# Performance work log

Hardware: AMD Instinct MI355X
Metric: run time of the kernel (lower is better)

Reference implementation:

```python
import jax, jax.numpy as jnp
import numpy as np

EPS = 1e-8  # torch F.cosine_similarity eps


def setup_inputs() -> dict:
    key = jax.random.key(0)
    B, CAP, CD, CTX = 32, 32768, 64, 64
    ks = jax.random.split(key, 9)
    inp = {
        "query_content": jax.random.normal(ks[0], (B, CD), jnp.float32),
        "query_context": jax.random.normal(ks[1], (B, CTX), jnp.float32),
        "memory_content": 0.1 * jax.random.normal(ks[2], (CAP, CD), jnp.float32),
        "memory_contexts": 0.1 * jax.random.normal(ks[3], (CAP, CTX), jnp.float32),
        "memory_freshness": jnp.ones((CAP,), jnp.float32),
        "W1": jax.random.normal(ks[4], (2 * CD, CD), jnp.float32) / np.sqrt(2 * CD),
        "b1": 0.01 * jax.random.normal(ks[5], (CD,), jnp.float32),
        "W2": jax.random.normal(ks[6], (CD, 1), jnp.float32) / np.sqrt(CD),
        "b2": 0.01 * jax.random.normal(ks[7], (1,), jnp.float32),
        "top_k": 16,
    }
    return inp


def reference(query_content, query_context, memory_content, memory_contexts,
              memory_freshness, W1, b1, W2, b2, top_k):
    B, CD = query_content.shape
    # similarity_calculator MLP over all (query, memory) pairs.
    # Linear on concat([q, m]) == q @ W1[:CD] + m @ W1[CD:]  (avoids the concat).
    q_part = query_content @ W1[:CD]            # [B, CD]
    m_part = memory_content @ W1[CD:]           # [CAP, CD]
    h = jax.nn.relu(q_part[:, None, :] + m_part[None, :, :] + b1)  # [B, CAP, CD]
    content_sim = jax.nn.sigmoid(jnp.einsum('bch,h->bc', h, W2[:, 0]) + b2[0])  # [B, CAP]

    # cosine similarity between query_context and each stored context
    qn = query_context / jnp.maximum(jnp.linalg.norm(query_context, axis=-1, keepdims=True), EPS)
    mn = memory_contexts / jnp.maximum(jnp.linalg.norm(memory_contexts, axis=-1, keepdims=True), EPS)
    context_sim = qn @ mn.T                      # [B, CAP]

    time_weights = memory_freshness              # time_mask is all-ones in source
    final = 0.5 * content_sim + 0.3 * context_sim + 0.2 * time_weights[None, :]

    top_similarities, top_indices = jax.lax.top_k(final, top_k)   # [B, k]
    retrieved_content = memory_content[top_indices]               # [B, k, CD]
    retrieved_time_weights = time_weights[top_indices]            # [B, k]
    return (retrieved_content, top_similarities, retrieved_time_weights)
```

## Files before the change

kernel.cpp:

```cpp
#include <hip/hip_runtime.h>
#include <math.h>

#define CAP   32768
#define NB    32
#define ROWS  64
#define NBLK  (CAP / ROWS)
#define TOPK  16
#define CEPS  1e-8f

#define PITCH 68
#define CHUNK 2048
#define NCHUNK (CAP / CHUNK)

#define WS_FINAL 0

__global__ __launch_bounds__(256) void score_kernel(
    const float* __restrict__ qc,
    const float* __restrict__ qctx,
    const float* __restrict__ mcont,
    const float* __restrict__ mctx,
    const float* __restrict__ fresh,
    const float* __restrict__ W1,
    const float* __restrict__ b1,
    const float* __restrict__ W2,
    const float* __restrict__ b2,
    float* __restrict__ ws)
{
    __shared__ float s_mp[ROWS * PITCH];
    __shared__ float s_qp[NB * PITCH];
    __shared__ float s_qn[NB * PITCH];
    __shared__ float s_out[NB * PITCH];
    __shared__ float s_base[ROWS];
    __shared__ float s_inv[ROWS];

    const int tid = threadIdx.x;
    const int C0 = blockIdx.x * ROWS;

    {
        const int b = tid >> 3, sl = tid & 7, j0 = sl * 8;
        const float* qrow = qc + b * 64;
        float acc[8];
        #pragma unroll
        for (int jj = 0; jj < 8; ++jj) acc[jj] = b1[j0 + jj];
        #pragma unroll 4
        for (int i = 0; i < 64; ++i) {
            float q = qrow[i];
            float4 wa = *(const float4*)&W1[i * 64 + j0];
            float4 wb = *(const float4*)&W1[i * 64 + j0 + 4];
            acc[0] = fmaf(q, wa.x, acc[0]); acc[1] = fmaf(q, wa.y, acc[1]);
            acc[2] = fmaf(q, wa.z, acc[2]); acc[3] = fmaf(q, wa.w, acc[3]);
            acc[4] = fmaf(q, wb.x, acc[4]); acc[5] = fmaf(q, wb.y, acc[5]);
            acc[6] = fmaf(q, wb.z, acc[6]); acc[7] = fmaf(q, wb.w, acc[7]);
        }
        #pragma unroll
        for (int jj = 0; jj < 8; ++jj) s_qp[b * PITCH + j0 + jj] = acc[jj];

        const float* xrow = qctx + b * 64;
        float ss = 0.f;
        #pragma unroll
        for (int i4 = 0; i4 < 16; ++i4) {
            float4 x = *(const float4*)&xrow[i4 * 4];
            ss = fmaf(x.x, x.x, ss); ss = fmaf(x.y, x.y, ss);
            ss = fmaf(x.z, x.z, ss); ss = fmaf(x.w, x.w, ss);
        }
        float rinv = 1.f / fmaxf(sqrtf(ss), CEPS);
        #pragma unroll
        for (int g = 0; g < 2; ++g) {
            float4 x = *(const float4*)&xrow[j0 + g * 4];
            s_qn[b * PITCH + j0 + g * 4 + 0] = x.x * rinv;
            s_qn[b * PITCH + j0 + g * 4 + 1] = x.y * rinv;
            s_qn[b * PITCH + j0 + g * 4 + 2] = x.z * rinv;
            s_qn[b * PITCH + j0 + g * 4 + 3] = x.w * rinv;
        }
    }
    if (tid < 64) {
        const float* xr = mctx + (size_t)(C0 + tid) * 64;
        float ss = 0.f;
        #pragma unroll
        for (int i4 = 0; i4 < 16; ++i4) {
            float4 x = *(const float4*)&xr[i4 * 4];
            ss = fmaf(x.x, x.x, ss); ss = fmaf(x.y, x.y, ss);
            ss = fmaf(x.z, x.z, ss); ss = fmaf(x.w, x.w, ss);
        }
        s_inv[tid]  = 0.3f / fmaxf(sqrtf(ss), CEPS);
        s_base[tid] = 0.2f * fresh[C0 + tid];
    }
    __syncthreads();

    {
        const int c_lo = tid & 15;
        const int j0 = (tid >> 4) * 4;
        float acc[4][4] = {{0.f}};
        const float* mrow = mcont + (size_t)(C0 + c_lo) * 64;
        #pragma unroll 4
        for (int i4 = 0; i4 < 16; ++i4) {
            float4 w0 = *(const float4*)&W1[(64 + i4 * 4 + 0) * 64 + j0];
            float4 w1r = *(const float4*)&W1[(64 + i4 * 4 + 1) * 64 + j0];
            float4 w2r = *(const float4*)&W1[(64 + i4 * 4 + 2) * 64 + j0];
            float4 w3r = *(const float4*)&W1[(64 + i4 * 4 + 3) * 64 + j0];
            #pragma unroll
            for (int ci = 0; ci < 4; ++ci) {
                float4 m = *(const float4*)&mrow[ci * 1024 + i4 * 4];
                acc[ci][0] = fmaf(m.x, w0.x, acc[ci][0]);
                acc[ci][1] = fmaf(m.x, w0.y, acc[ci][1]);
                acc[ci][2] = fmaf(m.x, w0.z, acc[ci][2]);
                acc[ci][3] = fmaf(m.x, w0.w, acc[ci][3]);
                acc[ci][0] = fmaf(m.y, w1r.x, acc[ci][0]);
                acc[ci][1] = fmaf(m.y, w1r.y, acc[ci][1]);
                acc[ci][2] = fmaf(m.y, w1r.z, acc[ci][2]);
                acc[ci][3] = fmaf(m.y, w1r.w, acc[ci][3]);
                acc[ci][0] = fmaf(m.z, w2r.x, acc[ci][0]);
                acc[ci][1] = fmaf(m.z, w2r.y, acc[ci][1]);
                acc[ci][2] = fmaf(m.z, w2r.z, acc[ci][2]);
                acc[ci][3] = fmaf(m.z, w2r.w, acc[ci][3]);
                acc[ci][0] = fmaf(m.w, w3r.x, acc[ci][0]);
                acc[ci][1] = fmaf(m.w, w3r.y, acc[ci][1]);
                acc[ci][2] = fmaf(m.w, w3r.z, acc[ci][2]);
                acc[ci][3] = fmaf(m.w, w3r.w, acc[ci][3]);
            }
        }
        #pragma unroll
        for (int ci = 0; ci < 4; ++ci)
            *(float4*)&s_mp[(c_lo + 16 * ci) * PITCH + j0] =
                make_float4(acc[ci][0], acc[ci][1], acc[ci][2], acc[ci][3]);
    }
    __syncthreads();

    const int bq = (tid & 15) << 1;
    const int cq = (tid >> 4) << 2;
    float a1[2][4] = {{0.f}}, a2[2][4] = {{0.f}};
    const float* mxb = mctx + (size_t)C0 * 64;

    #pragma unroll 4
    for (int j4 = 0; j4 < 16; ++j4) {
        const int jo = j4 * 4;
        float4 w2v = *(const float4*)(W2 + jo);
        float4 qp0 = *(const float4*)&s_qp[ bq      * PITCH + jo];
        float4 qp1 = *(const float4*)&s_qp[(bq + 1) * PITCH + jo];
        float4 qn0 = *(const float4*)&s_qn[ bq      * PITCH + jo];
        float4 qn1 = *(const float4*)&s_qn[(bq + 1) * PITCH + jo];
        #pragma unroll
        for (int ci = 0; ci < 4; ++ci) {
            float4 mv = *(const float4*)&s_mp[(cq + ci) * PITCH + jo];
            float4 xv = *(const float4*)&mxb[(cq + ci) * 64 + jo];
            a1[0][ci] = fmaf(fmaxf(qp0.x + mv.x, 0.f), w2v.x, a1[0][ci]);
            a1[0][ci] = fmaf(fmaxf(qp0.y + mv.y, 0.f), w2v.y, a1[0][ci]);
            a1[0][ci] = fmaf(fmaxf(qp0.z + mv.z, 0.f), w2v.z, a1[0][ci]);
            a1[0][ci] = fmaf(fmaxf(qp0.w + mv.w, 0.f), w2v.w, a1[0][ci]);
            a2[0][ci] = fmaf(qn0.x, xv.x, a2[0][ci]);
            a2[0][ci] = fmaf(qn0.y, xv.y, a2[0][ci]);
            a2[0][ci] = fmaf(qn0.z, xv.z, a2[0][ci]);
            a2[0][ci] = fmaf(qn0.w, xv.w, a2[0][ci]);
            a1[1][ci] = fmaf(fmaxf(qp1.x + mv.x, 0.f), w2v.x, a1[1][ci]);
            a1[1][ci] = fmaf(fmaxf(qp1.y + mv.y, 0.f), w2v.y, a1[1][ci]);
            a1[1][ci] = fmaf(fmaxf(qp1.z + mv.z, 0.f), w2v.z, a1[1][ci]);
            a1[1][ci] = fmaf(fmaxf(qp1.w + mv.w, 0.f), w2v.w, a1[1][ci]);
            a2[1][ci] = fmaf(qn1.x, xv.x, a2[1][ci]);
            a2[1][ci] = fmaf(qn1.y, xv.y, a2[1][ci]);
            a2[1][ci] = fmaf(qn1.z, xv.z, a2[1][ci]);
            a2[1][ci] = fmaf(qn1.w, xv.w, a2[1][ci]);
        }
    }

    const float b2v = b2[0];
    #pragma unroll
    for (int bi = 0; bi < 2; ++bi)
        #pragma unroll
        for (int ci = 0; ci < 4; ++ci) {
            const int b = bq + bi, c = cq + ci;
            float logit = a1[bi][ci] + b2v;
            float sig = 0.5f / (1.f + expf(-logit));
            s_out[b * PITCH + c] = sig + a2[bi][ci] * s_inv[c] + s_base[c];
        }
    __syncthreads();

    #pragma unroll
    for (int it = 0; it < 2; ++it) {
        int idx = it * 256 + tid;
        int b = idx >> 4, c4 = idx & 15;
        *(float4*)&ws[WS_FINAL + (size_t)b * CAP + C0 + c4 * 4] =
            *(const float4*)&s_out[b * PITCH + c4 * 4];
    }
}

__global__ __launch_bounds__(64) void topk_part1(float* __restrict__ ws)
{
    const int lane = threadIdx.x;
    const int b = blockIdx.y;
    float* row = ws + WS_FINAL + (size_t)b * CAP;
    const int cbase = blockIdx.x * CHUNK;

    float v[32];
    #pragma unroll
    for (int g = 0; g < 8; ++g) {
        float4 t = *(const float4*)&row[cbase + g * 256 + lane * 4];
        v[4 * g + 0] = t.x; v[4 * g + 1] = t.y;
        v[4 * g + 2] = t.z; v[4 * g + 3] = t.w;
    }

    float outv = 0.f;
    int   outi = 0;

    for (int k = 0; k < TOPK; ++k) {
        float bv = v[0]; int bj = 0;
        #pragma unroll
        for (int j = 1; j < 32; ++j)
            if (v[j] > bv) { bv = v[j]; bj = j; }
        int bi = cbase + (bj >> 2) * 256 + lane * 4 + (bj & 3);

        #pragma unroll
        for (int off = 1; off < 64; off <<= 1) {
            float ov = __shfl_xor(bv, off, 64);
            int   oi = __shfl_xor(bi, off, 64);
            if (ov > bv || (ov == bv && oi < bi)) { bv = ov; bi = oi; }
        }
        if (lane == k) { outv = bv; outi = bi; }

        int rel = bi - cbase;
        bool mine = (((rel >> 2) & 63) == lane);
        int wj = ((rel >> 8) << 2) | (rel & 3);
        #pragma unroll
        for (int j = 0; j < 32; ++j)
            if (mine && wj == j) v[j] = -INFINITY;
    }

    if (lane < TOPK) {
        row[cbase + lane]        = outv;
        row[cbase + TOPK + lane] = __int_as_float(outi);
    }
}

__global__ __launch_bounds__(64) void topk_part2(
    const float* __restrict__ mcont,
    const float* __restrict__ fresh,
    const float* __restrict__ ws,
    float* __restrict__ out)
{
    const int lane = threadIdx.x;
    const int b = blockIdx.x;
    const float* row = ws + WS_FINAL + (size_t)b * CAP;

    float* out_content = out;
    float* out_sim     = out + NB * TOPK * 64;
    float* out_tw      = out + NB * TOPK * 64 + NB * TOPK;

    const int chunk = lane & 15;
    const int s0 = lane >> 4;
    float v[4]; int iv[4];
    #pragma unroll
    for (int s = 0; s < 4; ++s) {
        v[s]  = row[chunk * CHUNK + s0 + 4 * s];
        iv[s] = __float_as_int(row[chunk * CHUNK + TOPK + s0 + 4 * s]);
    }

    float wval = 0.f; int widx = 0;
    for (int k = 0; k < TOPK; ++k) {
        float bv = v[0]; int bi = iv[0];
        #pragma unroll
        for (int s = 1; s < 4; ++s)
            if (v[s] > bv || (v[s] == bv && iv[s] < bi)) { bv = v[s]; bi = iv[s]; }
        #pragma unroll
        for (int off = 1; off < 64; off <<= 1) {
            float ov = __shfl_xor(bv, off, 64);
            int   oi = __shfl_xor(bi, off, 64);
            if (ov > bv || (ov == bv && oi < bi)) { bv = ov; bi = oi; }
        }
        if (lane == k) { wval = bv; widx = bi; }
        #pragma unroll
        for (int s = 0; s < 4; ++s)
            if (iv[s] == bi) v[s] = -INFINITY;
    }

    if (lane < TOPK) {
        out_sim[b * TOPK + lane] = wval;
        out_tw [b * TOPK + lane] = fresh[widx];
    }

    #pragma unroll
    for (int r = 0; r < TOPK; ++r) {
        int wi = __shfl(widx, r, 64);
        out_content[(size_t)b * TOPK * 64 + r * 64 + lane] =
            mcont[(size_t)wi * 64 + lane];
    }
}

extern "C" void kernel_launch(void* const* d_in, const int* in_sizes, int n_in,
                              void* d_out, int out_size, void* d_ws, size_t ws_size,
                              hipStream_t stream) {
    const float* qc    = (const float*)d_in[0];
    const float* qctx  = (const float*)d_in[1];
    const float* mcont = (const float*)d_in[2];
    const float* mctx  = (const float*)d_in[3];
    const float* fresh = (const float*)d_in[4];
    const float* W1    = (const float*)d_in[5];
    const float* b1    = (const float*)d_in[6];
    const float* W2    = (const float*)d_in[7];
    const float* b2    = (const float*)d_in[8];
    float* out = (float*)d_out;
    float* ws  = (float*)d_ws;

    score_kernel<<<NBLK, 256, 0, stream>>>(qc, qctx, mcont, mctx, fresh,
                                           W1, b1, W2, b2, ws);
    topk_part1<<<dim3(NCHUNK, NB), 64, 0, stream>>>(ws);
    topk_part2<<<NB, 64, 0, stream>>>(mcont, fresh, ws, out);
}
```

Before: 153.4 us.

## Hoist query projections into prep kernel and stage memory rows in LDS

Adds a small prep kernel that computes the query projection and normalized query context once, instead of every score block recomputing them for all 32 queries. The score kernel now stages the memory content tile in LDS, spreads the context-norm work across all threads, and stores the projected memory transposed so the ReLU-MLP loop reads float4 vectors along the memory dimension. Final results are written straight from registers as float4, which removes the output staging buffer and one barrier. The cost is an extra kernel launch and a trip through global workspace for the query data.

After: 137.4 us. -10.4%, faster.

```diff
diff --git a/kernel.cpp b/kernel.cpp
--- a/kernel.cpp
+++ b/kernel.cpp
@@ -12,86 +12,96 @@
 #define CHUNK 2048
 #define NCHUNK (CAP / CHUNK)
 
-#define WS_FINAL 0
-
-__global__ __launch_bounds__(256) void score_kernel(
+#define WS_QP    0
+#define WS_QN    2048
+#define WS_FINAL 4096
+
+__global__ __launch_bounds__(64) void prep_kernel(
     const float* __restrict__ qc,
     const float* __restrict__ qctx,
+    const float* __restrict__ W1,
+    const float* __restrict__ b1,
+    float* __restrict__ ws)
+{
+    const int b = blockIdx.x;
+    const int j = threadIdx.x;
+
+    float a0 = b1[j], a1 = 0.f, a2 = 0.f, a3 = 0.f;
+    #pragma unroll
+    for (int i = 0; i < 64; i += 4) {
+        a0 = fmaf(qc[b * 64 + i + 0], W1[(i + 0) * 64 + j], a0);
+        a1 = fmaf(qc[b * 64 + i + 1], W1[(i + 1) * 64 + j], a1);
+        a2 = fmaf(qc[b * 64 + i + 2], W1[(i + 2) * 64 + j], a2);
+        a3 = fmaf(qc[b * 64 + i + 3], W1[(i + 3) * 64 + j], a3);
+    }
+    ws[WS_QP + b * 64 + j] = (a0 + a1) + (a2 + a3);
+
+    float x = qctx[b * 64 + j];
+    float ss = x * x;
+    ss += __shfl_xor(ss, 1,  64);
+    ss += __shfl_xor(ss, 2,  64);
+    ss += __shfl_xor(ss, 4,  64);
+    ss += __shfl_xor(ss, 8,  64);
+    ss += __shfl_xor(ss, 16, 64);
+    ss += __shfl_xor(ss, 32, 64);
+    ws[WS_QN + b * 64 + j] = x / fmaxf(sqrtf(ss), CEPS);
+}
+
+__global__ __launch_bounds__(256) void score_kernel(
     const float* __restrict__ mcont,
     const float* __restrict__ mctx,
     const float* __restrict__ fresh,
     const float* __restrict__ W1,
-    const float* __restrict__ b1,
     const float* __restrict__ W2,
     const float* __restrict__ b2,
     float* __restrict__ ws)
 {
-    __shared__ float s_mp[ROWS * PITCH];
+    __shared__ float s_mc[ROWS * PITCH];
     __shared__ float s_qp[NB * PITCH];
     __shared__ float s_qn[NB * PITCH];
-    __shared__ float s_out[NB * PITCH];
     __shared__ float s_base[ROWS];
     __shared__ float s_inv[ROWS];
 
     const int tid = threadIdx.x;
     const int C0 = blockIdx.x * ROWS;
 
+    const float4* g_mc = (const float4*)(mcont + (size_t)C0 * 64);
+    #pragma unroll
+    for (int t = tid; t < ROWS * 16; t += 256) {
+        int r = t >> 4, c4 = t & 15;
+        *(float4*)&s_mc[r * PITCH + c4 * 4] = g_mc[t];
+    }
+    const float4* g_qp = (const float4*)(ws + WS_QP);
+    const float4* g_qn = (const float4*)(ws + WS_QN);
+    #pragma unroll
+    for (int t = tid; t < NB * 16; t += 256) {
+        int r = t >> 4, c4 = t & 15;
+        *(float4*)&s_qp[r * PITCH + c4 * 4] = g_qp[t];
+        *(float4*)&s_qn[r * PITCH + c4 * 4] = g_qn[t];
+    }
     {
-        const int b = tid >> 3, sl = tid & 7, j0 = sl * 8;
-        const float* qrow = qc + b * 64;
-        float acc[8];
-        #pragma unroll
-        for (int jj = 0; jj < 8; ++jj) acc[jj] = b1[j0 + jj];
-        #pragma unroll 4
-        for (int i = 0; i < 64; ++i) {
-            float q = qrow[i];
-            float4 wa = *(const float4*)&W1[i * 64 + j0];
-            float4 wb = *(const float4*)&W1[i * 64 + j0 + 4];
-            acc[0] = fmaf(q, wa.x, acc[0]); acc[1] = fmaf(q, wa.y, acc[1]);
-            acc[2] = fmaf(q, wa.z, acc[2]); acc[3] = fmaf(q, wa.w, acc[3]);
-            acc[4] = fmaf(q, wb.x, acc[4]); acc[5] = fmaf(q, wb.y, acc[5]);
-            acc[6] = fmaf(q, wb.z, acc[6]); acc[7] = fmaf(q, wb.w, acc[7]);
-        }
-        #pragma unroll
-        for (int jj = 0; jj < 8; ++jj) s_qp[b * PITCH + j0 + jj] = acc[jj];
-
-        const float* xrow = qctx + b * 64;
+        const int r = tid >> 2, q = tid & 3;
+        const float* xr = mctx + (size_t)(C0 + r) * 64 + q * 16;
         float ss = 0.f;
         #pragma unroll
-        for (int i4 = 0; i4 < 16; ++i4) {
-            float4 x = *(const float4*)&xrow[i4 * 4];
+        for (int i = 0; i < 4; ++i) {
+            float4 x = *(const float4*)&xr[i * 4];
             ss = fmaf(x.x, x.x, ss); ss = fmaf(x.y, x.y, ss);
             ss = fmaf(x.z, x.z, ss); ss = fmaf(x.w, x.w, ss);
         }
-        float rinv = 1.f / fmaxf(sqrtf(ss), CEPS);
-        #pragma unroll
-        for (int g = 0; g < 2; ++g) {
-            float4 x = *(const float4*)&xrow[j0 + g * 4];
-            s_qn[b * PITCH + j0 + g * 4 + 0] = x.x * rinv;
-            s_qn[b * PITCH + j0 + g * 4 + 1] = x.y * rinv;
-            s_qn[b * PITCH + j0 + g * 4 + 2] = x.z * rinv;
-            s_qn[b * PITCH + j0 + g * 4 + 3] = x.w * rinv;
-        }
-    }
-    if (tid < 64) {
-        const float* xr = mctx + (size_t)(C0 + tid) * 64;
-        float ss = 0.f;
-        #pragma unroll
-        for (int i4 = 0; i4 < 16; ++i4) {
-            float4 x = *(const float4*)&xr[i4 * 4];
-            ss = fmaf(x.x, x.x, ss); ss = fmaf(x.y, x.y, ss);
-            ss = fmaf(x.z, x.z, ss); ss = fmaf(x.w, x.w, ss);
-        }
-        s_inv[tid]  = 0.3f / fmaxf(sqrtf(ss), CEPS);
-        s_base[tid] = 0.2f * fresh[C0 + tid];
+        ss += __shfl_xor(ss, 1, 64);
+        ss += __shfl_xor(ss, 2, 64);
+        if (q == 0) {
+            s_inv[r]  = 0.3f / fmaxf(sqrtf(ss), CEPS);
+            s_base[r] = 0.2f * fresh[C0 + r];
+        }
     }
     __syncthreads();
 
+    const int c_lo = tid & 15;
+    const int j0 = (tid >> 4) * 4;
     {
-        const int c_lo = tid & 15;
-        const int j0 = (tid >> 4) * 4;
         float acc[4][4] = {{0.f}};
-        const float* mrow = mcont + (size_t)(C0 + c_lo) * 64;
         #pragma unroll 4
         for (int i4 = 0; i4 < 16; ++i4) {
             float4 w0 = *(const float4*)&W1[(64 + i4 * 4 + 0) * 64 + j0];
@@ -100,7 +110,7 @@
             float4 w3r = *(const float4*)&W1[(64 + i4 * 4 + 3) * 64 + j0];
             #pragma unroll
             for (int ci = 0; ci < 4; ++ci) {
-                float4 m = *(const float4*)&mrow[ci * 1024 + i4 * 4];
+                float4 m = *(const float4*)&s_mc[(c_lo + 16 * ci) * PITCH + i4 * 4];
                 acc[ci][0] = fmaf(m.x, w0.x, acc[ci][0]);
                 acc[ci][1] = fmaf(m.x, w0.y, acc[ci][1]);
                 acc[ci][2] = fmaf(m.x, w0.z, acc[ci][2]);
@@ -119,16 +129,21 @@
                 acc[ci][3] = fmaf(m.w, w3r.w, acc[ci][3]);
             }
         }
-        #pragma unroll
-        for (int ci = 0; ci < 4; ++ci)
-            *(float4*)&s_mp[(c_lo + 16 * ci) * PITCH + j0] =
-                make_float4(acc[ci][0], acc[ci][1], acc[ci][2], acc[ci][3]);
+        __syncthreads();
+        #pragma unroll
+        for (int jj = 0; jj < 4; ++jj)
+            #pragma unroll
+            for (int ci = 0; ci < 4; ++ci)
+                s_mc[(j0 + jj) * PITCH + c_lo + 16 * ci] = acc[ci][jj];
     }
     __syncthreads();
 
     const int bq = (tid & 15) << 1;
     const int cq = (tid >> 4) << 2;
-    float a1[2][4] = {{0.f}}, a2[2][4] = {{0.f}};
+    float4 a1v[2];
+    a1v[0] = make_float4(0.f, 0.f, 0.f, 0.f);
+    a1v[1] = make_float4(0.f, 0.f, 0.f, 0.f);
+    float a2[2][4] = {{0.f}};
     const float* mxb = mctx + (size_t)C0 * 64;
 
     #pragma unroll 4
@@ -139,22 +154,39 @@
         float4 qp1 = *(const float4*)&s_qp[(bq + 1) * PITCH + jo];
         float4 qn0 = *(const float4*)&s_qn[ bq      * PITCH + jo];
         float4 qn1 = *(const float4*)&s_qn[(bq + 1) * PITCH + jo];
+        float4 m0 = *(const float4*)&s_mc[(jo + 0) * PITCH + cq];
+        float4 m1 = *(const float4*)&s_mc[(jo + 1) * PITCH + cq];
+        float4 m2 = *(const float4*)&s_mc[(jo + 2) * PITCH + cq];
+        float4 m3 = *(const float4*)&s_mc[(jo + 3) * PITCH + cq];
+
+        #pragma unroll
+        for (int bi = 0; bi < 2; ++bi) {
+            float4 qp = bi ? qp1 : qp0;
+            float4& av = a1v[bi];
+            av.x = fmaf(fmaxf(qp.x + m0.x, 0.f), w2v.x, av.x);
+            av.y = fmaf(fmaxf(qp.x + m0.y, 0.f), w2v.x, av.y);
+            av.z = fmaf(fmaxf(qp.x + m0.z, 0.f), w2v.x, av.z);
+            av.w = fmaf(fmaxf(qp.x + m0.w, 0.f), w2v.x, av.w);
+            av.x = fmaf(fmaxf(qp.y + m1.x, 0.f), w2v.y, av.x);
+            av.y = fmaf(fmaxf(qp.y + m1.y, 0.f), w2v.y, av.y);
+            av.z = fmaf(fmaxf(qp.y + m1.z, 0.f), w2v.y, av.z);
+            av.w = fmaf(fmaxf(qp.y + m1.w, 0.f), w2v.y, av.w);
+            av.x = fmaf(fmaxf(qp.z + m2.x, 0.f), w2v.z, av.x);
+            av.y = fmaf(fmaxf(qp.z + m2.y, 0.f), w2v.z, av.y);
+            av.z = fmaf(fmaxf(qp.z + m2.z, 0.f), w2v.z, av.z);
+            av.w = fmaf(fmaxf(qp.z + m2.w, 0.f), w2v.z, av.w);
+            av.x = fmaf(fmaxf(qp.w + m3.x, 0.f), w2v.w, av.x);
+            av.y = fmaf(fmaxf(qp.w + m3.y, 0.f), w2v.w, av.y);
+            av.z = fmaf(fmaxf(qp.w + m3.z, 0.f), w2v.w, av.z);
+            av.w = fmaf(fmaxf(qp.w + m3.w, 0.f), w2v.w, av.w);
+        }
         #pragma unroll
         for (int ci = 0; ci < 4; ++ci) {
-            float4 mv = *(const float4*)&s_mp[(cq + ci) * PITCH + jo];
             float4 xv = *(const float4*)&mxb[(cq + ci) * 64 + jo];
-            a1[0][ci] = fmaf(fmaxf(qp0.x + mv.x, 0.f), w2v.x, a1[0][ci]);
-            a1[0][ci] = fmaf(fmaxf(qp0.y + mv.y, 0.f), w2v.y, a1[0][ci]);
-            a1[0][ci] = fmaf(fmaxf(qp0.z + mv.z, 0.f), w2v.z, a1[0][ci]);
-            a1[0][ci] = fmaf(fmaxf(qp0.w + mv.w, 0.f), w2v.w, a1[0][ci]);
             a2[0][ci] = fmaf(qn0.x, xv.x, a2[0][ci]);
             a2[0][ci] = fmaf(qn0.y, xv.y, a2[0][ci]);
             a2[0][ci] = fmaf(qn0.z, xv.z, a2[0][ci]);
             a2[0][ci] = fmaf(qn0.w, xv.w, a2[0][ci]);
-            a1[1][ci] = fmaf(fmaxf(qp1.x + mv.x, 0.f), w2v.x, a1[1][ci]);
-            a1[1][ci] = fmaf(fmaxf(qp1.y + mv.y, 0.f), w2v.y, a1[1][ci]);
-            a1[1][ci] = fmaf(fmaxf(qp1.z + mv.z, 0.f), w2v.z, a1[1][ci]);
-            a1[1][ci] = fmaf(fmaxf(qp1.w + mv.w, 0.f), w2v.w, a1[1][ci]);
             a2[1][ci] = fmaf(qn1.x, xv.x, a2[1][ci]);
             a2[1][ci] = fmaf(qn1.y, xv.y, a2[1][ci]);
             a2[1][ci] = fmaf(qn1.z, xv.z, a2[1][ci]);
@@ -163,23 +195,16 @@
     }
 
     const float b2v = b2[0];
-    #pragma unroll
-    for (int bi = 0; bi < 2; ++bi)
-        #pragma unroll
-        for (int ci = 0; ci < 4; ++ci) {
-            const int b = bq + bi, c = cq + ci;
-            float logit = a1[bi][ci] + b2v;
-            float sig = 0.5f / (1.f + expf(-logit));
-            s_out[b * PITCH + c] = sig + a2[bi][ci] * s_inv[c] + s_base[c];
-        }
-    __syncthreads();
-
-    #pragma unroll
-    for (int it = 0; it < 2; ++it) {
-        int idx = it * 256 + tid;
-        int b = idx >> 4, c4 = idx & 15;
-        *(float4*)&ws[WS_FINAL + (size_t)b * CAP + C0 + c4 * 4] =
-            *(const float4*)&s_out[b * PITCH + c4 * 4];
+    float4 inv4  = *(const float4*)&s_inv[cq];
+    float4 base4 = *(const float4*)&s_base[cq];
+    #pragma unroll
+    for (int bi = 0; bi < 2; ++bi) {
+        float4 r;
+        r.x = 0.5f / (1.f + expf(-(a1v[bi].x + b2v))) + a2[bi][0] * inv4.x + base4.x;
+        r.y = 0.5f / (1.f + expf(-(a1v[bi].y + b2v))) + a2[bi][1] * inv4.y + base4.y;
+        r.z = 0.5f / (1.f + expf(-(a1v[bi].z + b2v))) + a2[bi][2] * inv4.z + base4.z;
+        r.w = 0.5f / (1.f + expf(-(a1v[bi].w + b2v))) + a2[bi][3] * inv4.w + base4.w;
+        *(float4*)&ws[WS_FINAL + (size_t)(bq + bi) * CAP + C0 + cq] = r;
     }
 }
 
@@ -299,8 +324,8 @@
     float* out = (float*)d_out;
     float* ws  = (float*)d_ws;
 
-    score_kernel<<<NBLK, 256, 0, stream>>>(qc, qctx, mcont, mctx, fresh,
-                                           W1, b1, W2, b2, ws);
+    prep_kernel<<<NB, 64, 0, stream>>>(qc, qctx, W1, b1, ws);
+    score_kernel<<<NBLK, 256, 0, stream>>>(mcont, mctx, fresh, W1, W2, b2, ws);
     topk_part1<<<dim3(NCHUNK, NB), 64, 0, stream>>>(ws);
     topk_part2<<<NB, 64, 0, stream>>>(mcont, fresh, ws, out);
 }
```
